# Optimization experiments

Measured on AMD Instinct MI355X. Metric: run time of the kernel, lower is better.

Reference implementation:

```python
import jax, jax.numpy as jnp
import numpy as np

B, N, D_NODE, D_EDGE, D_GRAPH = 2, 1024, 128, 16, 128
MID, OUT = 64, 128


def _linear_params(key, fan_in, fan_out):
    # haiku Linear default: truncated-normal(stddev=1/sqrt(fan_in)) weight, zero bias
    w = jax.random.normal(key, (fan_in, fan_out), dtype=jnp.float32) / np.sqrt(fan_in)
    b = jnp.zeros((fan_out,), dtype=jnp.float32)
    return w, b


def setup_inputs() -> dict:
    key = jax.random.key(0)
    ks = jax.random.split(key, 12)
    features = jax.random.normal(ks[0], (B, N, D_NODE), dtype=jnp.float32)
    e_features = jax.random.normal(ks[1], (B, N, N, D_EDGE), dtype=jnp.float32)
    g_features = jax.random.normal(ks[2], (B, D_GRAPH), dtype=jnp.float32)
    adj = jax.random.randint(ks[3], (B, N, N), 0, 2).astype(jnp.float32)
    # ensure self-loops so every row has at least one valid neighbor
    adj = jnp.maximum(adj, jnp.eye(N, dtype=jnp.float32)[None])
    Wm, bm = _linear_params(ks[4], D_NODE, OUT)
    Wskip, bskip = _linear_params(ks[5], D_NODE, OUT)
    W1, b1 = _linear_params(ks[6], D_NODE, MID)
    W2, b2 = _linear_params(ks[7], D_NODE, MID)
    We, be = _linear_params(ks[8], D_EDGE, MID)
    Wg, bg = _linear_params(ks[9], D_GRAPH, MID)
    Wa, ba = _linear_params(ks[10], MID, 1)
    return dict(features=features, e_features=e_features, g_features=g_features,
                adj=adj, Wm=Wm, bm=bm, Wskip=Wskip, bskip=bskip,
                W1=W1, b1=b1, W2=W2, b2=b2, We=We, be=be, Wg=Wg, bg=bg,
                Wa=Wa, ba=ba)


def reference(features, e_features, g_features, adj,
              Wm, bm, Wskip, bskip, W1, b1, W2, b2, We, be, Wg, bg, Wa, ba):
    # bias mask: 0 where edge exists, -1e9 where not
    bias_mat = (adj - 1.0) * 1e9  # (b,n,n)

    values = features @ Wm + bm          # (b,n,out)
    pre_att_1 = features @ W1 + b1       # (b,n,mid) -> per-target j
    pre_att_2 = features @ W2 + b2       # (b,n,mid) -> per-source i
    pre_att_e = e_features @ We + be     # (b,n,n,mid)
    pre_att_g = g_features @ Wg + bg     # (b,mid)

    # pre_att[b,i,j] = p1[b,j] + p2[b,i] + pe[b,i,j] + pg[b]
    pre_att = (pre_att_1[:, None, :, :] + pre_att_2[:, :, None, :]
               + pre_att_e + pre_att_g[:, None, None, :])  # (b,n,n,mid)

    logits = jnp.squeeze(jax.nn.leaky_relu(pre_att) @ Wa + ba, axis=-1)  # (b,n,n)
    coefs = jax.nn.softmax(logits + bias_mat, axis=-1)                   # (b,n,n)

    ret = jnp.matmul(coefs, values)       # (b,n,out)
    ret = ret + (features @ Wskip + bskip)  # residual
    return jax.nn.relu(ret)               # activation=relu
```

## Files before the change

### kernel.cpp

```cpp
#include <hip/hip_runtime.h>
#include <hip/hip_bf16.h>
#include <cstdint>

#define B_   2
#define N_   1024
#define DN_  128
#define DE_  16
#define DG_  128
#define MID_ 64
#define OUT_ 128
#define TI_  4
#define PR_ROWS 4

typedef short bf16x8 __attribute__((ext_vector_type(8)));
typedef float f32x4  __attribute__((ext_vector_type(4)));

__device__ inline short f2bf(float f) {
    union { float f; unsigned u; } v; v.f = f;
    unsigned r = v.u + 0x7FFFu + ((v.u >> 16) & 1u);
    return (short)(unsigned short)(r >> 16);
}

__device__ inline unsigned pk2(float lo, float hi) {
    union { __hip_bfloat162 h; unsigned u; } p;
    p.h = __float22bfloat162_rn(make_float2(lo, hi));
    return p.u;
}

__global__ void __launch_bounds__(384) prep_all(
    const float* __restrict__ features, const float* __restrict__ g_features,
    const float* __restrict__ Wm, const float* __restrict__ bm,
    const float* __restrict__ Wskip, const float* __restrict__ bskip,
    const float* __restrict__ W1, const float* __restrict__ b1,
    const float* __restrict__ W2, const float* __restrict__ b2,
    const float* __restrict__ We, const float* __restrict__ be,
    const float* __restrict__ Wg, const float* __restrict__ bg,
    float* __restrict__ values, float* __restrict__ skipo,
    float* __restrict__ P1x, float* __restrict__ p2,
    float* __restrict__ pg, short* __restrict__ We_frag)
{
    const int t   = threadIdx.x;
    const int blk = blockIdx.x;

    if (blk == 512) {
        for (int e = t; e < 4 * 64 * 8; e += 384) {
            const int c    = e >> 9;
            const int lane = (e >> 3) & 63;
            const int j    = e & 7;
            const int quad = lane >> 4, s = lane & 15;
            short v = 0;
            if (quad < 2) v = f2bf(We[(quad * 8 + j) * MID_ + c * 16 + s]);
            We_frag[e] = v;
        }
        return;
    }
    if (blk == 513) {
        if (t < MID_) {
            float a0 = bg[t], a1 = bg[t];
            for (int k = 0; k < DG_; ++k) {
                const float w = Wg[k * MID_ + t];
                a0 += g_features[k] * w;
                a1 += g_features[DG_ + k] * w;
            }
            pg[t] = a0; pg[MID_ + t] = a1;
        }
        return;
    }

    const int r0 = blk * PR_ROWS;
    __shared__ float feat[PR_ROWS][DN_];
    for (int idx = t; idx < PR_ROWS * DN_; idx += 384)
        feat[idx >> 7][idx & 127] = features[(size_t)r0 * DN_ + idx];
    __syncthreads();

    const float* W; int c, stride; float base; float* outp; int ostride;
    if (t < 128) {
        W = Wm;    c = t;       stride = OUT_; base = bm[c];
        outp = values + (size_t)r0 * OUT_ + c; ostride = OUT_;
    } else if (t < 256) {
        W = Wskip; c = t - 128; stride = OUT_; base = bskip[c];
        outp = skipo + (size_t)r0 * OUT_ + c;  ostride = OUT_;
    } else if (t < 320) {
        W = W1;    c = t - 256; stride = MID_; base = b1[c] + be[c];
        outp = P1x + (size_t)r0 * MID_ + c;    ostride = MID_;
    } else {
        W = W2;    c = t - 320; stride = MID_; base = b2[c];
        outp = p2 + (size_t)r0 * MID_ + c;     ostride = MID_;
    }

    float acc[PR_ROWS] = {};
    for (int k = 0; k < DN_; ++k) {
        const float w = W[k * stride + c];
        #pragma unroll
        for (int q = 0; q < PR_ROWS; ++q) acc[q] += feat[q][k] * w;
    }
    #pragma unroll
    for (int q = 0; q < PR_ROWS; ++q) outp[q * ostride] = acc[q] + base;
}

__global__ void __launch_bounds__(256) gat_main(
    const float* __restrict__ e_features, const float* __restrict__ adj,
    const short* __restrict__ We_frag, const float* __restrict__ Wa,
    const float* __restrict__ values, const float* __restrict__ skipo,
    const float* __restrict__ P1x, const float* __restrict__ p2,
    const float* __restrict__ pg, float* __restrict__ out)
{
    const int t    = threadIdx.x;
    const int wv   = t >> 6;
    const int l    = t & 63;
    const int quad = l >> 4;
    const int s    = l & 15;
    const int r    = blockIdx.x;
    const int b    = (r >> 2) & 1;
    const int i0   = (((r >> 3) << 2) | (r & 3)) * TI_;

    __shared__ float lgP[TI_][N_];
    __shared__ float redv[TI_][16][36];
    __shared__ float sinv[TI_];

    bf16x8 bfr[4];
    float  wa_r[4], p2i[TI_][4];
    #pragma unroll
    for (int c = 0; c < 4; ++c) {
        bfr[c]  = *(const bf16x8*)&We_frag[(c * 64 + l) * 8];
        wa_r[c] = Wa[c * 16 + s];
        const float pgc = pg[b * MID_ + c * 16 + s];
        #pragma unroll
        for (int ii = 0; ii < TI_; ++ii)
            p2i[ii][c] = p2[((size_t)(b * N_ + i0 + ii)) * MID_ + c * 16 + s] + pgc;
    }
    const size_t erow0 = (size_t)(b * N_ + i0) * N_;

    float4 eA[TI_][2];
    if (quad < 2) {
        #pragma unroll
        for (int ii = 0; ii < TI_; ++ii) {
            const float* ep = &e_features[(erow0 + (size_t)ii * N_ + wv * 16 + s) * DE_ + quad * 8];
            eA[ii][0] = *(const float4*)ep;
            eA[ii][1] = *(const float4*)(ep + 4);
        }
    }
    for (int it = 0; it < 16; ++it) {
        const int tile = wv + it * 4;
        const int j0   = tile * 16;

        unsigned af[TI_][4];
        #pragma unroll
        for (int ii = 0; ii < TI_; ++ii) {
            if (quad < 2) {
                af[ii][0] = pk2(eA[ii][0].x, eA[ii][0].y);
                af[ii][1] = pk2(eA[ii][0].z, eA[ii][0].w);
                af[ii][2] = pk2(eA[ii][1].x, eA[ii][1].y);
                af[ii][3] = pk2(eA[ii][1].z, eA[ii][1].w);
            } else {
                af[ii][0] = af[ii][1] = af[ii][2] = af[ii][3] = 0u;
            }
        }
        if (it < 15) {
            const int jn = (tile + 4) * 16;
            if (quad < 2) {
                #pragma unroll
                for (int ii = 0; ii < TI_; ++ii) {
                    const float* ep = &e_features[(erow0 + (size_t)ii * N_ + jn + s) * DE_ + quad * 8];
                    eA[ii][0] = *(const float4*)ep;
                    eA[ii][1] = *(const float4*)(ep + 4);
                }
            }
        }
        float base[4][4];
        {
            const float* pb = &P1x[((size_t)(b * N_) + j0 + quad * 4) * MID_ + s];
            #pragma unroll
            for (int c = 0; c < 4; ++c)
                #pragma unroll
                for (int rr = 0; rr < 4; ++rr)
                    base[c][rr] = pb[rr * MID_ + c * 16];
        }
        #pragma unroll
        for (int ii = 0; ii < TI_; ++ii) {
            union { unsigned u[4]; bf16x8 v; } a;
            a.u[0] = af[ii][0]; a.u[1] = af[ii][1];
            a.u[2] = af[ii][2]; a.u[3] = af[ii][3];
            f32x4 acc[4];
            #pragma unroll
            for (int c = 0; c < 4; ++c) {
                acc[c] = (f32x4){0.f, 0.f, 0.f, 0.f};
                acc[c] = __builtin_amdgcn_mfma_f32_16x16x32_bf16(a.v, bfr[c], acc[c], 0, 0, 0);
            }
            float tt[4];
            #pragma unroll
            for (int rr = 0; rr < 4; ++rr) {
                float x0 = acc[0][rr] + base[0][rr] + p2i[ii][0];
                float x1 = acc[1][rr] + base[1][rr] + p2i[ii][1];
                float x2 = acc[2][rr] + base[2][rr] + p2i[ii][2];
                float x3 = acc[3][rr] + base[3][rr] + p2i[ii][3];
                x0 = fmaxf(x0, 0.01f * x0);
                x1 = fmaxf(x1, 0.01f * x1);
                x2 = fmaxf(x2, 0.01f * x2);
                x3 = fmaxf(x3, 0.01f * x3);
                tt[rr] = x0 * wa_r[0] + x1 * wa_r[1] + x2 * wa_r[2] + x3 * wa_r[3];
            }
            #pragma unroll
            for (int o = 1; o < 16; o <<= 1) {
                tt[0] += __shfl_xor(tt[0], o);
                tt[1] += __shfl_xor(tt[1], o);
                tt[2] += __shfl_xor(tt[2], o);
                tt[3] += __shfl_xor(tt[3], o);
            }
            if (s < 4) lgP[ii][j0 + quad * 4 + s] = tt[s];
        }
    }
    __syncthreads();

    {
        const size_t arb = (size_t)(b * N_ + i0 + wv) * N_;
        float4 lv[4], av[4];
        #pragma unroll
        for (int q = 0; q < 4; ++q) {
            lv[q] = *(const float4*)&lgP[wv][l * 4 + 256 * q];
            av[q] = *(const float4*)&adj[arb + l * 4 + 256 * q];
        }
        const float NEG = -3.4e38f;
        float m = NEG;
        #pragma unroll
        for (int q = 0; q < 4; ++q) {
            m = fmaxf(m, av[q].x > 0.f ? lv[q].x : NEG);
            m = fmaxf(m, av[q].y > 0.f ? lv[q].y : NEG);
            m = fmaxf(m, av[q].z > 0.f ? lv[q].z : NEG);
            m = fmaxf(m, av[q].w > 0.f ? lv[q].w : NEG);
        }
        #pragma unroll
        for (int o = 1; o < 64; o <<= 1) m = fmaxf(m, __shfl_xor(m, o));
        float sum = 0.f;
        #pragma unroll
        for (int q = 0; q < 4; ++q) {
            float4 e4;
            e4.x = av[q].x > 0.f ? __expf(lv[q].x - m) : 0.f;
            e4.y = av[q].y > 0.f ? __expf(lv[q].y - m) : 0.f;
            e4.z = av[q].z > 0.f ? __expf(lv[q].z - m) : 0.f;
            e4.w = av[q].w > 0.f ? __expf(lv[q].w - m) : 0.f;
            *(float4*)&lgP[wv][l * 4 + 256 * q] = e4;
            sum += (e4.x + e4.y) + (e4.z + e4.w);
        }
        #pragma unroll
        for (int o = 1; o < 64; o <<= 1) sum += __shfl_xor(sum, o);
        if (l == 0) sinv[wv] = 1.0f / sum;
    }
    __syncthreads();

    const int cg = l & 15, jp = l >> 4, ch0 = cg * 8;
    float acc[TI_][8] = {};
    const float* vb = values + (size_t)b * N_ * OUT_ + ch0;
    for (int k = 0; k < 64; ++k) {
        const int j = wv * 4 + jp + k * 16;
        float cw[TI_];
        #pragma unroll
        for (int ii = 0; ii < TI_; ++ii) cw[ii] = lgP[ii][j];
        const float* vp = vb + (size_t)j * OUT_;
        const float4 v0 = *(const float4*)vp;
        const float4 v1 = *(const float4*)(vp + 4);
        const float vv[8] = {v0.x, v0.y, v0.z, v0.w, v1.x, v1.y, v1.z, v1.w};
        #pragma unroll
        for (int ii = 0; ii < TI_; ++ii)
            #pragma unroll
            for (int kk = 0; kk < 8; ++kk)
                acc[ii][kk] += cw[ii] * vv[kk];
    }
    #pragma unroll
    for (int ii = 0; ii < TI_; ++ii)
        #pragma unroll
        for (int kk = 0; kk < 8; ++kk) {
            acc[ii][kk] += __shfl_xor(acc[ii][kk], 16);
            acc[ii][kk] += __shfl_xor(acc[ii][kk], 32);
        }
    if (l < 16) {
        #pragma unroll
        for (int ii = 0; ii < TI_; ++ii)
            #pragma unroll
            for (int q = 0; q < 2; ++q) {
                float4 w4 = make_float4(acc[ii][q * 4], acc[ii][q * 4 + 1],
                                        acc[ii][q * 4 + 2], acc[ii][q * 4 + 3]);
                *(float4*)&redv[wv][l][ii * 8 + q * 4] = w4;
            }
    }
    __syncthreads();
    {
        const int ch = t & 127, g = ch >> 3, kk = ch & 7;
        const int iib = t >> 7;
        #pragma unroll
        for (int p = 0; p < 2; ++p) {
            const int ii = iib + p * 2;
            const float sum = redv[0][g][ii * 8 + kk] + redv[1][g][ii * 8 + kk]
                            + redv[2][g][ii * 8 + kk] + redv[3][g][ii * 8 + kk];
            const size_t ob = ((size_t)(b * N_ + i0 + ii)) * OUT_ + ch;
            out[ob] = fmaxf(sum * sinv[ii] + skipo[ob], 0.f);
        }
    }
}

extern "C" void kernel_launch(void* const* d_in, const int* in_sizes, int n_in,
                              void* d_out, int out_size, void* d_ws, size_t ws_size,
                              hipStream_t stream) {
    const float* features   = (const float*)d_in[0];
    const float* e_features = (const float*)d_in[1];
    const float* g_features = (const float*)d_in[2];
    const float* adj        = (const float*)d_in[3];
    const float* Wm    = (const float*)d_in[4];
    const float* bm    = (const float*)d_in[5];
    const float* Wskip = (const float*)d_in[6];
    const float* bskip = (const float*)d_in[7];
    const float* W1    = (const float*)d_in[8];
    const float* b1    = (const float*)d_in[9];
    const float* W2    = (const float*)d_in[10];
    const float* b2    = (const float*)d_in[11];
    const float* We    = (const float*)d_in[12];
    const float* be    = (const float*)d_in[13];
    const float* Wg    = (const float*)d_in[14];
    const float* bg    = (const float*)d_in[15];
    const float* Wa    = (const float*)d_in[16];
    float* out = (float*)d_out;

    float* ws      = (float*)d_ws;
    float* values  = ws;
    float* skipo   = ws + 262144;
    float* P1x     = ws + 524288;
    float* p2      = ws + 655360;
    float* pg      = ws + 786432;
    short* We_frag = (short*)(ws + 786560);

    prep_all<<<B_ * N_ / PR_ROWS + 2, 384, 0, stream>>>(
        features, g_features, Wm, bm, Wskip, bskip, W1, b1, W2, b2,
        We, be, Wg, bg, values, skipo, P1x, p2, pg, We_frag);
    gat_main<<<B_ * N_ / TI_, 256, 0, stream>>>(
        e_features, adj, We_frag, Wa, values, skipo, P1x, p2, pg, out);
}
```

Measured before the change: 297.9 us.

## Halve rows per block and restructure softmax and aggregation across waves

```diff
diff --git a/kernel.cpp b/kernel.cpp
--- a/kernel.cpp
+++ b/kernel.cpp
@@ -9,7 +9,7 @@
 #define DG_  128
 #define MID_ 64
 #define OUT_ 128
-#define TI_  4
+#define TI_  2
 #define PR_ROWS 4
 
 typedef short bf16x8 __attribute__((ext_vector_type(8)));
@@ -112,11 +112,11 @@
     const int s    = l & 15;
     const int r    = blockIdx.x;
     const int b    = (r >> 2) & 1;
-    const int i0   = (((r >> 3) << 2) | (r & 3)) * TI_;
+    const int i0   = ((((r >> 3) << 2) | (r & 3))) * TI_;
 
     __shared__ float lgP[TI_][N_];
-    __shared__ float redv[TI_][16][36];
-    __shared__ float sinv[TI_];
+    __shared__ float4 redc[TI_][4][32];
+    __shared__ float smax[4], ssum[4];
 
     bf16x8 bfr[4];
     float  wa_r[4], p2i[TI_][4];
@@ -184,20 +184,18 @@
             f32x4 acc[4];
             #pragma unroll
             for (int c = 0; c < 4; ++c) {
-                acc[c] = (f32x4){0.f, 0.f, 0.f, 0.f};
+                #pragma unroll
+                for (int rr = 0; rr < 4; ++rr)
+                    acc[c][rr] = base[c][rr] + p2i[ii][c];
                 acc[c] = __builtin_amdgcn_mfma_f32_16x16x32_bf16(a.v, bfr[c], acc[c], 0, 0, 0);
             }
             float tt[4];
             #pragma unroll
             for (int rr = 0; rr < 4; ++rr) {
-                float x0 = acc[0][rr] + base[0][rr] + p2i[ii][0];
-                float x1 = acc[1][rr] + base[1][rr] + p2i[ii][1];
-                float x2 = acc[2][rr] + base[2][rr] + p2i[ii][2];
-                float x3 = acc[3][rr] + base[3][rr] + p2i[ii][3];
-                x0 = fmaxf(x0, 0.01f * x0);
-                x1 = fmaxf(x1, 0.01f * x1);
-                x2 = fmaxf(x2, 0.01f * x2);
-                x3 = fmaxf(x3, 0.01f * x3);
+                float x0 = acc[0][rr]; x0 = fmaxf(x0, 0.01f * x0);
+                float x1 = acc[1][rr]; x1 = fmaxf(x1, 0.01f * x1);
+                float x2 = acc[2][rr]; x2 = fmaxf(x2, 0.01f * x2);
+                float x3 = acc[3][rr]; x3 = fmaxf(x3, 0.01f * x3);
                 tt[rr] = x0 * wa_r[0] + x1 * wa_r[1] + x2 * wa_r[2] + x3 * wa_r[3];
             }
             #pragma unroll
@@ -213,88 +211,82 @@
     __syncthreads();
 
     {
-        const size_t arb = (size_t)(b * N_ + i0 + wv) * N_;
-        float4 lv[4], av[4];
-        #pragma unroll
-        for (int q = 0; q < 4; ++q) {
-            lv[q] = *(const float4*)&lgP[wv][l * 4 + 256 * q];
-            av[q] = *(const float4*)&adj[arb + l * 4 + 256 * q];
-        }
+        const int tt8 = (t & 127) * 8;
+        const int p   = t >> 7;
+        const size_t arb = (size_t)(b * N_ + i0 + p) * N_;
+        float4 lv0 = *(const float4*)&lgP[p][tt8];
+        float4 lv1 = *(const float4*)&lgP[p][tt8 + 4];
+        float4 av0 = *(const float4*)&adj[arb + tt8];
+        float4 av1 = *(const float4*)&adj[arb + tt8 + 4];
         const float NEG = -3.4e38f;
         float m = NEG;
-        #pragma unroll
-        for (int q = 0; q < 4; ++q) {
-            m = fmaxf(m, av[q].x > 0.f ? lv[q].x : NEG);
-            m = fmaxf(m, av[q].y > 0.f ? lv[q].y : NEG);
-            m = fmaxf(m, av[q].z > 0.f ? lv[q].z : NEG);
-            m = fmaxf(m, av[q].w > 0.f ? lv[q].w : NEG);
-        }
+        m = fmaxf(m, av0.x > 0.f ? lv0.x : NEG);
+        m = fmaxf(m, av0.y > 0.f ? lv0.y : NEG);
+        m = fmaxf(m, av0.z > 0.f ? lv0.z : NEG);
+        m = fmaxf(m, av0.w > 0.f ? lv0.w : NEG);
+        m = fmaxf(m, av1.x > 0.f ? lv1.x : NEG);
+        m = fmaxf(m, av1.y > 0.f ? lv1.y : NEG);
+        m = fmaxf(m, av1.z > 0.f ? lv1.z : NEG);
+        m = fmaxf(m, av1.w > 0.f ? lv1.w : NEG);
         #pragma unroll
         for (int o = 1; o < 64; o <<= 1) m = fmaxf(m, __shfl_xor(m, o));
-        float sum = 0.f;
-        #pragma unroll
-        for (int q = 0; q < 4; ++q) {
-            float4 e4;
-            e4.x = av[q].x > 0.f ? __expf(lv[q].x - m) : 0.f;
-            e4.y = av[q].y > 0.f ? __expf(lv[q].y - m) : 0.f;
-            e4.z = av[q].z > 0.f ? __expf(lv[q].z - m) : 0.f;
-            e4.w = av[q].w > 0.f ? __expf(lv[q].w - m) : 0.f;
-            *(float4*)&lgP[wv][l * 4 + 256 * q] = e4;
-            sum += (e4.x + e4.y) + (e4.z + e4.w);
-        }
+        if (l == 0) smax[wv] = m;
+        __syncthreads();
+        m = fmaxf(smax[p * 2], smax[p * 2 + 1]);
+        float4 e0, e1;
+        e0.x = av0.x > 0.f ? __expf(lv0.x - m) : 0.f;
+        e0.y = av0.y > 0.f ? __expf(lv0.y - m) : 0.f;
+        e0.z = av0.z > 0.f ? __expf(lv0.z - m) : 0.f;
+        e0.w = av0.w > 0.f ? __expf(lv0.w - m) : 0.f;
+        e1.x = av1.x > 0.f ? __expf(lv1.x - m) : 0.f;
+        e1.y = av1.y > 0.f ? __expf(lv1.y - m) : 0.f;
+        e1.z = av1.z > 0.f ? __expf(lv1.z - m) : 0.f;
+        e1.w = av1.w > 0.f ? __expf(lv1.w - m) : 0.f;
+        *(float4*)&lgP[p][tt8]     = e0;
+        *(float4*)&lgP[p][tt8 + 4] = e1;
+        float sum = ((e0.x + e0.y) + (e0.z + e0.w)) + ((e1.x + e1.y) + (e1.z + e1.w));
         #pragma unroll
         for (int o = 1; o < 64; o <<= 1) sum += __shfl_xor(sum, o);
-        if (l == 0) sinv[wv] = 1.0f / sum;
+        if (l == 0) ssum[wv] = sum;
+        __syncthreads();
+    }
+
+    {
+        const int cg = t & 31;
+        const int jp = t >> 5;
+        const float* vb = values + (size_t)b * N_ * OUT_ + cg * 4;
+        float4 a0 = make_float4(0.f, 0.f, 0.f, 0.f);
+        float4 a1 = make_float4(0.f, 0.f, 0.f, 0.f);
+        for (int j = jp; j < N_; j += 8) {
+            const float w0 = lgP[0][j];
+            const float w1 = lgP[1][j];
+            const float4 v = *(const float4*)&vb[(size_t)j * OUT_];
+            a0.x += w0 * v.x; a0.y += w0 * v.y; a0.z += w0 * v.z; a0.w += w0 * v.w;
+            a1.x += w1 * v.x; a1.y += w1 * v.y; a1.z += w1 * v.z; a1.w += w1 * v.w;
+        }
+        a0.x += __shfl_xor(a0.x, 32); a0.y += __shfl_xor(a0.y, 32);
+        a0.z += __shfl_xor(a0.z, 32); a0.w += __shfl_xor(a0.w, 32);
+        a1.x += __shfl_xor(a1.x, 32); a1.y += __shfl_xor(a1.y, 32);
+        a1.z += __shfl_xor(a1.z, 32); a1.w += __shfl_xor(a1.w, 32);
+        if (l < 32) {
+            redc[0][wv][l] = a0;
+            redc[1][wv][l] = a1;
+        }
     }
     __syncthreads();
-
-    const int cg = l & 15, jp = l >> 4, ch0 = cg * 8;
-    float acc[TI_][8] = {};
-    const float* vb = values + (size_t)b * N_ * OUT_ + ch0;
-    for (int k = 0; k < 64; ++k) {
-        const int j = wv * 4 + jp + k * 16;
-        float cw[TI_];
-        #pragma unroll
-        for (int ii = 0; ii < TI_; ++ii) cw[ii] = lgP[ii][j];
-        const float* vp = vb + (size_t)j * OUT_;
-        const float4 v0 = *(const float4*)vp;
-        const float4 v1 = *(const float4*)(vp + 4);
-        const float vv[8] = {v0.x, v0.y, v0.z, v0.w, v1.x, v1.y, v1.z, v1.w};
-        #pragma unroll
-        for (int ii = 0; ii < TI_; ++ii)
-            #pragma unroll
-            for (int kk = 0; kk < 8; ++kk)
-                acc[ii][kk] += cw[ii] * vv[kk];
-    }
-    #pragma unroll
-    for (int ii = 0; ii < TI_; ++ii)
-        #pragma unroll
-        for (int kk = 0; kk < 8; ++kk) {
-            acc[ii][kk] += __shfl_xor(acc[ii][kk], 16);
-            acc[ii][kk] += __shfl_xor(acc[ii][kk], 32);
-        }
-    if (l < 16) {
-        #pragma unroll
-        for (int ii = 0; ii < TI_; ++ii)
-            #pragma unroll
-            for (int q = 0; q < 2; ++q) {
-                float4 w4 = make_float4(acc[ii][q * 4], acc[ii][q * 4 + 1],
-                                        acc[ii][q * 4 + 2], acc[ii][q * 4 + 3]);
-                *(float4*)&redv[wv][l][ii * 8 + q * 4] = w4;
-            }
-    }
-    __syncthreads();
-    {
-        const int ch = t & 127, g = ch >> 3, kk = ch & 7;
-        const int iib = t >> 7;
-        #pragma unroll
-        for (int p = 0; p < 2; ++p) {
-            const int ii = iib + p * 2;
-            const float sum = redv[0][g][ii * 8 + kk] + redv[1][g][ii * 8 + kk]
-                            + redv[2][g][ii * 8 + kk] + redv[3][g][ii * 8 + kk];
-            const size_t ob = ((size_t)(b * N_ + i0 + ii)) * OUT_ + ch;
-            out[ob] = fmaxf(sum * sinv[ii] + skipo[ob], 0.f);
-        }
+    if (t < 64) {
+        const int ch4 = t & 31, p = t >> 5;
+        const float4 r0 = redc[p][0][ch4], r1 = redc[p][1][ch4];
+        const float4 r2 = redc[p][2][ch4], r3 = redc[p][3][ch4];
+        const float inv = 1.0f / (ssum[p * 2] + ssum[p * 2 + 1]);
+        const size_t ob = ((size_t)(b * N_ + i0 + p)) * OUT_ + ch4 * 4;
+        const float4 sk = *(const float4*)&skipo[ob];
+        float4 o;
+        o.x = fmaxf((r0.x + r1.x + r2.x + r3.x) * inv + sk.x, 0.f);
+        o.y = fmaxf((r0.y + r1.y + r2.y + r3.y) * inv + sk.y, 0.f);
+        o.z = fmaxf((r0.z + r1.z + r2.z + r3.z) * inv + sk.z, 0.f);
+        o.w = fmaxf((r0.w + r1.w + r2.w + r3.w) * inv + sk.w, 0.f);
+        *(float4*)&out[ob] = o;
     }
 }
 
```

New measurement: 349.4 us. 1.17x slower.

## Double gat_main block to 512 threads, splitting tiles and softmax across 8 waves

Applied to the files above, without the earlier changes.

```diff
diff --git a/kernel.cpp b/kernel.cpp
--- a/kernel.cpp
+++ b/kernel.cpp
@@ -98,7 +98,7 @@
     for (int q = 0; q < PR_ROWS; ++q) outp[q * ostride] = acc[q] + base;
 }
 
-__global__ void __launch_bounds__(256) gat_main(
+__global__ void __launch_bounds__(512, 4) gat_main(
     const float* __restrict__ e_features, const float* __restrict__ adj,
     const short* __restrict__ We_frag, const float* __restrict__ Wa,
     const float* __restrict__ values, const float* __restrict__ skipo,
@@ -115,8 +115,8 @@
     const int i0   = (((r >> 3) << 2) | (r & 3)) * TI_;
 
     __shared__ float lgP[TI_][N_];
-    __shared__ float redv[TI_][16][36];
-    __shared__ float sinv[TI_];
+    __shared__ float redv[8][16][36];
+    __shared__ float smax[8], ssum[8];
 
     bf16x8 bfr[4];
     float  wa_r[4], p2i[TI_][4];
@@ -140,8 +140,8 @@
             eA[ii][1] = *(const float4*)(ep + 4);
         }
     }
-    for (int it = 0; it < 16; ++it) {
-        const int tile = wv + it * 4;
+    for (int it = 0; it < 8; ++it) {
+        const int tile = wv + it * 8;
         const int j0   = tile * 16;
 
         unsigned af[TI_][4];
@@ -156,8 +156,8 @@
                 af[ii][0] = af[ii][1] = af[ii][2] = af[ii][3] = 0u;
             }
         }
-        if (it < 15) {
-            const int jn = (tile + 4) * 16;
+        if (it < 7) {
+            const int jn = (tile + 8) * 16;
             if (quad < 2) {
                 #pragma unroll
                 for (int ii = 0; ii < TI_; ++ii) {
@@ -184,20 +184,18 @@
             f32x4 acc[4];
             #pragma unroll
             for (int c = 0; c < 4; ++c) {
-                acc[c] = (f32x4){0.f, 0.f, 0.f, 0.f};
+                #pragma unroll
+                for (int rr = 0; rr < 4; ++rr)
+                    acc[c][rr] = base[c][rr] + p2i[ii][c];
                 acc[c] = __builtin_amdgcn_mfma_f32_16x16x32_bf16(a.v, bfr[c], acc[c], 0, 0, 0);
             }
             float tt[4];
             #pragma unroll
             for (int rr = 0; rr < 4; ++rr) {
-                float x0 = acc[0][rr] + base[0][rr] + p2i[ii][0];
-                float x1 = acc[1][rr] + base[1][rr] + p2i[ii][1];
-                float x2 = acc[2][rr] + base[2][rr] + p2i[ii][2];
-                float x3 = acc[3][rr] + base[3][rr] + p2i[ii][3];
-                x0 = fmaxf(x0, 0.01f * x0);
-                x1 = fmaxf(x1, 0.01f * x1);
-                x2 = fmaxf(x2, 0.01f * x2);
-                x3 = fmaxf(x3, 0.01f * x3);
+                float x0 = acc[0][rr]; x0 = fmaxf(x0, 0.01f * x0);
+                float x1 = acc[1][rr]; x1 = fmaxf(x1, 0.01f * x1);
+                float x2 = acc[2][rr]; x2 = fmaxf(x2, 0.01f * x2);
+                float x3 = acc[3][rr]; x3 = fmaxf(x3, 0.01f * x3);
                 tt[rr] = x0 * wa_r[0] + x1 * wa_r[1] + x2 * wa_r[2] + x3 * wa_r[3];
             }
             #pragma unroll
@@ -213,88 +211,96 @@
     __syncthreads();
 
     {
-        const size_t arb = (size_t)(b * N_ + i0 + wv) * N_;
-        float4 lv[4], av[4];
-        #pragma unroll
-        for (int q = 0; q < 4; ++q) {
-            lv[q] = *(const float4*)&lgP[wv][l * 4 + 256 * q];
-            av[q] = *(const float4*)&adj[arb + l * 4 + 256 * q];
-        }
+        const int p = wv & 3, h = wv >> 2;
+        const int o8 = h * 512 + l * 8;
+        const size_t arb = (size_t)(b * N_ + i0 + p) * N_;
+        float4 lv0 = *(const float4*)&lgP[p][o8];
+        float4 lv1 = *(const float4*)&lgP[p][o8 + 4];
+        float4 av0 = *(const float4*)&adj[arb + o8];
+        float4 av1 = *(const float4*)&adj[arb + o8 + 4];
         const float NEG = -3.4e38f;
         float m = NEG;
-        #pragma unroll
-        for (int q = 0; q < 4; ++q) {
-            m = fmaxf(m, av[q].x > 0.f ? lv[q].x : NEG);
-            m = fmaxf(m, av[q].y > 0.f ? lv[q].y : NEG);
-            m = fmaxf(m, av[q].z > 0.f ? lv[q].z : NEG);
-            m = fmaxf(m, av[q].w > 0.f ? lv[q].w : NEG);
-        }
+        m = fmaxf(m, av0.x > 0.f ? lv0.x : NEG);
+        m = fmaxf(m, av0.y > 0.f ? lv0.y : NEG);
+        m = fmaxf(m, av0.z > 0.f ? lv0.z : NEG);
+        m = fmaxf(m, av0.w > 0.f ? lv0.w : NEG);
+        m = fmaxf(m, av1.x > 0.f ? lv1.x : NEG);
+        m = fmaxf(m, av1.y > 0.f ? lv1.y : NEG);
+        m = fmaxf(m, av1.z > 0.f ? lv1.z : NEG);
+        m = fmaxf(m, av1.w > 0.f ? lv1.w : NEG);
         #pragma unroll
         for (int o = 1; o < 64; o <<= 1) m = fmaxf(m, __shfl_xor(m, o));
-        float sum = 0.f;
-        #pragma unroll
-        for (int q = 0; q < 4; ++q) {
-            float4 e4;
-            e4.x = av[q].x > 0.f ? __expf(lv[q].x - m) : 0.f;
-            e4.y = av[q].y > 0.f ? __expf(lv[q].y - m) : 0.f;
-            e4.z = av[q].z > 0.f ? __expf(lv[q].z - m) : 0.f;
-            e4.w = av[q].w > 0.f ? __expf(lv[q].w - m) : 0.f;
-            *(float4*)&lgP[wv][l * 4 + 256 * q] = e4;
-            sum += (e4.x + e4.y) + (e4.z + e4.w);
-        }
+        if (l == 0) smax[wv] = m;
+        __syncthreads();
+        m = fmaxf(smax[p], smax[p + 4]);
+        float4 e0, e1;
+        e0.x = av0.x > 0.f ? __expf(lv0.x - m) : 0.f;
+        e0.y = av0.y > 0.f ? __expf(lv0.y - m) : 0.f;
+        e0.z = av0.z > 0.f ? __expf(lv0.z - m) : 0.f;
+        e0.w = av0.w > 0.f ? __expf(lv0.w - m) : 0.f;
+        e1.x = av1.x > 0.f ? __expf(lv1.x - m) : 0.f;
+        e1.y = av1.y > 0.f ? __expf(lv1.y - m) : 0.f;
+        e1.z = av1.z > 0.f ? __expf(lv1.z - m) : 0.f;
+        e1.w = av1.w > 0.f ? __expf(lv1.w - m) : 0.f;
+        *(float4*)&lgP[p][o8]     = e0;
+        *(float4*)&lgP[p][o8 + 4] = e1;
+        float sum = ((e0.x + e0.y) + (e0.z + e0.w)) + ((e1.x + e1.y) + (e1.z + e1.w));
         #pragma unroll
         for (int o = 1; o < 64; o <<= 1) sum += __shfl_xor(sum, o);
-        if (l == 0) sinv[wv] = 1.0f / sum;
-    }
-    __syncthreads();
-
-    const int cg = l & 15, jp = l >> 4, ch0 = cg * 8;
-    float acc[TI_][8] = {};
-    const float* vb = values + (size_t)b * N_ * OUT_ + ch0;
-    for (int k = 0; k < 64; ++k) {
-        const int j = wv * 4 + jp + k * 16;
-        float cw[TI_];
-        #pragma unroll
-        for (int ii = 0; ii < TI_; ++ii) cw[ii] = lgP[ii][j];
-        const float* vp = vb + (size_t)j * OUT_;
-        const float4 v0 = *(const float4*)vp;
-        const float4 v1 = *(const float4*)(vp + 4);
-        const float vv[8] = {v0.x, v0.y, v0.z, v0.w, v1.x, v1.y, v1.z, v1.w};
+        if (l == 0) ssum[wv] = sum;
+        __syncthreads();
+    }
+
+    {
+        const int cg  = l & 15;
+        const int jp  = (wv << 2) | (l >> 4);
+        const int ch0 = cg * 8;
+        float acc[TI_][8] = {};
+        const float* vb = values + (size_t)b * N_ * OUT_ + ch0;
+        for (int k = 0; k < 32; ++k) {
+            const int j = jp + k * 32;
+            float cw[TI_];
+            #pragma unroll
+            for (int ii = 0; ii < TI_; ++ii) cw[ii] = lgP[ii][j];
+            const float* vp = vb + (size_t)j * OUT_;
+            const float4 v0 = *(const float4*)vp;
+            const float4 v1 = *(const float4*)(vp + 4);
+            const float vv[8] = {v0.x, v0.y, v0.z, v0.w, v1.x, v1.y, v1.z, v1.w};
+            #pragma unroll
+            for (int ii = 0; ii < TI_; ++ii)
+                #pragma unroll
+                for (int kk = 0; kk < 8; ++kk)
+                    acc[ii][kk] += cw[ii] * vv[kk];
+        }
         #pragma unroll
         for (int ii = 0; ii < TI_; ++ii)
             #pragma unroll
-            for (int kk = 0; kk < 8; ++kk)
-                acc[ii][kk] += cw[ii] * vv[kk];
-    }
-    #pragma unroll
-    for (int ii = 0; ii < TI_; ++ii)
-        #pragma unroll
-        for (int kk = 0; kk < 8; ++kk) {
-            acc[ii][kk] += __shfl_xor(acc[ii][kk], 16);
-            acc[ii][kk] += __shfl_xor(acc[ii][kk], 32);
-        }
-    if (l < 16) {
-        #pragma unroll
-        for (int ii = 0; ii < TI_; ++ii)
-            #pragma unroll
-            for (int q = 0; q < 2; ++q) {
-                float4 w4 = make_float4(acc[ii][q * 4], acc[ii][q * 4 + 1],
-                                        acc[ii][q * 4 + 2], acc[ii][q * 4 + 3]);
-                *(float4*)&redv[wv][l][ii * 8 + q * 4] = w4;
-            }
+            for (int kk = 0; kk < 8; ++kk) {
+                acc[ii][kk] += __shfl_xor(acc[ii][kk], 16);
+                acc[ii][kk] += __shfl_xor(acc[ii][kk], 32);
+            }
+        if (l < 16) {
+            #pragma unroll
+            for (int ii = 0; ii < TI_; ++ii)
+                #pragma unroll
+                for (int q = 0; q < 2; ++q) {
+                    float4 w4 = make_float4(acc[ii][q * 4], acc[ii][q * 4 + 1],
+                                            acc[ii][q * 4 + 2], acc[ii][q * 4 + 3]);
+                    *(float4*)&redv[wv][l][ii * 8 + q * 4] = w4;
+                }
+        }
     }
     __syncthreads();
     {
-        const int ch = t & 127, g = ch >> 3, kk = ch & 7;
-        const int iib = t >> 7;
-        #pragma unroll
-        for (int p = 0; p < 2; ++p) {
-            const int ii = iib + p * 2;
-            const float sum = redv[0][g][ii * 8 + kk] + redv[1][g][ii * 8 + kk]
-                            + redv[2][g][ii * 8 + kk] + redv[3][g][ii * 8 + kk];
-            const size_t ob = ((size_t)(b * N_ + i0 + ii)) * OUT_ + ch;
-            out[ob] = fmaxf(sum * sinv[ii] + skipo[ob], 0.f);
-        }
+        const int ii = t >> 7;
+        const int ch = t & 127;
+        const int g  = ch >> 3, kk = ch & 7;
+        float sum = 0.f;
+        #pragma unroll
+        for (int w = 0; w < 8; ++w) sum += redv[w][g][ii * 8 + kk];
+        const float inv = 1.0f / (ssum[ii] + ssum[ii + 4]);
+        const size_t ob = ((size_t)(b * N_ + i0 + ii)) * OUT_ + ch;
+        out[ob] = fmaxf(sum * inv + skipo[ob], 0.f);
     }
 }
 
@@ -331,6 +337,6 @@
     prep_all<<<B_ * N_ / PR_ROWS + 2, 384, 0, stream>>>(
         features, g_features, Wm, bm, Wskip, bskip, W1, b1, W2, b2,
         We, be, Wg, bg, values, skipo, P1x, p2, pg, We_frag);
-    gat_main<<<B_ * N_ / TI_, 256, 0, stream>>>(
+    gat_main<<<B_ * N_ / TI_, 512, 0, stream>>>(
         e_features, adj, We_frag, Wa, values, skipo, P1x, p2, pg, out);
 }
```

Measured after the change: 429.9 us. +44.3%, slower.

## Split GAT into logits kernel with 4x more blocks and separate softmax-aggregate kernel

Applied to the files above, without the earlier changes.

```diff
diff --git a/kernel.cpp b/kernel.cpp
--- a/kernel.cpp
+++ b/kernel.cpp
@@ -98,7 +98,231 @@
     for (int q = 0; q < PR_ROWS; ++q) outp[q * ostride] = acc[q] + base;
 }
 
-__global__ void __launch_bounds__(256) gat_main(
+__global__ void __launch_bounds__(256) gat_logits(
+    const float* __restrict__ e_features, const float* __restrict__ adj,
+    const short* __restrict__ We_frag, const float* __restrict__ Wa,
+    const float* __restrict__ P1x, const float* __restrict__ p2,
+    const float* __restrict__ pg, float* __restrict__ lgG)
+{
+    const int t     = threadIdx.x;
+    const int wv    = t >> 6;
+    const int l     = t & 63;
+    const int quad  = l >> 4;
+    const int s     = l & 15;
+    const int r     = blockIdx.x;
+    const int jc    = r & 3;
+    const int b     = (r >> 2) & 1;
+    const int i0    = (r >> 3) * TI_;
+    const int jbase = jc * 256;
+
+    __shared__ float lgL[TI_][256];
+
+    bf16x8 bfr[4];
+    float  wa_r[4], p2i[TI_][4];
+    #pragma unroll
+    for (int c = 0; c < 4; ++c) {
+        bfr[c]  = *(const bf16x8*)&We_frag[(c * 64 + l) * 8];
+        wa_r[c] = Wa[c * 16 + s];
+        const float pgc = pg[b * MID_ + c * 16 + s];
+        #pragma unroll
+        for (int ii = 0; ii < TI_; ++ii)
+            p2i[ii][c] = p2[((size_t)(b * N_ + i0 + ii)) * MID_ + c * 16 + s] + pgc;
+    }
+    const size_t erow0 = (size_t)(b * N_ + i0) * N_;
+
+    float4 eA[TI_][2];
+    if (quad < 2) {
+        #pragma unroll
+        for (int ii = 0; ii < TI_; ++ii) {
+            const float* ep = &e_features[(erow0 + (size_t)ii * N_ + jbase + wv * 16 + s) * DE_ + quad * 8];
+            eA[ii][0] = *(const float4*)ep;
+            eA[ii][1] = *(const float4*)(ep + 4);
+        }
+    }
+    for (int it = 0; it < 4; ++it) {
+        const int j0 = jbase + (wv + it * 4) * 16;
+
+        unsigned af[TI_][4];
+        #pragma unroll
+        for (int ii = 0; ii < TI_; ++ii) {
+            if (quad < 2) {
+                af[ii][0] = pk2(eA[ii][0].x, eA[ii][0].y);
+                af[ii][1] = pk2(eA[ii][0].z, eA[ii][0].w);
+                af[ii][2] = pk2(eA[ii][1].x, eA[ii][1].y);
+                af[ii][3] = pk2(eA[ii][1].z, eA[ii][1].w);
+            } else {
+                af[ii][0] = af[ii][1] = af[ii][2] = af[ii][3] = 0u;
+            }
+        }
+        if (it < 3) {
+            const int jn = jbase + (wv + (it + 1) * 4) * 16;
+            if (quad < 2) {
+                #pragma unroll
+                for (int ii = 0; ii < TI_; ++ii) {
+                    const float* ep = &e_features[(erow0 + (size_t)ii * N_ + jn + s) * DE_ + quad * 8];
+                    eA[ii][0] = *(const float4*)ep;
+                    eA[ii][1] = *(const float4*)(ep + 4);
+                }
+            }
+        }
+        float base[4][4];
+        {
+            const float* pb = &P1x[((size_t)(b * N_) + j0 + quad * 4) * MID_ + s];
+            #pragma unroll
+            for (int c = 0; c < 4; ++c)
+                #pragma unroll
+                for (int rr = 0; rr < 4; ++rr)
+                    base[c][rr] = pb[rr * MID_ + c * 16];
+        }
+        #pragma unroll
+        for (int ii = 0; ii < TI_; ++ii) {
+            union { unsigned u[4]; bf16x8 v; } a;
+            a.u[0] = af[ii][0]; a.u[1] = af[ii][1];
+            a.u[2] = af[ii][2]; a.u[3] = af[ii][3];
+            f32x4 acc[4];
+            #pragma unroll
+            for (int c = 0; c < 4; ++c) {
+                #pragma unroll
+                for (int rr = 0; rr < 4; ++rr)
+                    acc[c][rr] = base[c][rr] + p2i[ii][c];
+                acc[c] = __builtin_amdgcn_mfma_f32_16x16x32_bf16(a.v, bfr[c], acc[c], 0, 0, 0);
+            }
+            float tt[4];
+            #pragma unroll
+            for (int rr = 0; rr < 4; ++rr) {
+                float x0 = acc[0][rr]; x0 = fmaxf(x0, 0.01f * x0);
+                float x1 = acc[1][rr]; x1 = fmaxf(x1, 0.01f * x1);
+                float x2 = acc[2][rr]; x2 = fmaxf(x2, 0.01f * x2);
+                float x3 = acc[3][rr]; x3 = fmaxf(x3, 0.01f * x3);
+                tt[rr] = x0 * wa_r[0] + x1 * wa_r[1] + x2 * wa_r[2] + x3 * wa_r[3];
+            }
+            #pragma unroll
+            for (int o = 1; o < 16; o <<= 1) {
+                tt[0] += __shfl_xor(tt[0], o);
+                tt[1] += __shfl_xor(tt[1], o);
+                tt[2] += __shfl_xor(tt[2], o);
+                tt[3] += __shfl_xor(tt[3], o);
+            }
+            if (s < 4) lgL[ii][j0 - jbase + quad * 4 + s] = tt[s];
+        }
+    }
+    __syncthreads();
+
+    {
+        const int   ii  = t >> 6;
+        const int   jl  = (t & 63) * 4;
+        const size_t row = (size_t)(b * N_ + i0 + ii);
+        float4 lg4 = make_float4(lgL[ii][jl], lgL[ii][jl + 1],
+                                 lgL[ii][jl + 2], lgL[ii][jl + 3]);
+        const float4 a4 = *(const float4*)&adj[row * N_ + jbase + jl];
+        const float NEG = -3.4e38f;
+        lg4.x = a4.x > 0.f ? lg4.x : NEG;
+        lg4.y = a4.y > 0.f ? lg4.y : NEG;
+        lg4.z = a4.z > 0.f ? lg4.z : NEG;
+        lg4.w = a4.w > 0.f ? lg4.w : NEG;
+        *(float4*)&lgG[row * N_ + jbase + jl] = lg4;
+    }
+}
+
+__global__ void __launch_bounds__(256) gat_out(
+    const float* __restrict__ lgG, const float* __restrict__ values,
+    const float* __restrict__ skipo, float* __restrict__ out)
+{
+    const int t  = threadIdx.x;
+    const int wv = t >> 6;
+    const int l  = t & 63;
+    const int r  = blockIdx.x;
+    const int b  = (r >> 2) & 1;
+    const int i0 = (((r >> 3) << 2) | (r & 3)) * TI_;
+
+    __shared__ float lgP[TI_][N_];
+    __shared__ float redv[4][16][36];
+    __shared__ float sinv[TI_];
+
+    #pragma unroll
+    for (int ii = 0; ii < TI_; ++ii)
+        *(float4*)&lgP[ii][t * 4] =
+            *(const float4*)&lgG[(size_t)(b * N_ + i0 + ii) * N_ + t * 4];
+    __syncthreads();
+
+    {
+        float v[16];
+        float m = -3.4e38f;
+        #pragma unroll
+        for (int q = 0; q < 16; ++q) {
+            v[q] = lgP[wv][l + 64 * q];
+            m = fmaxf(m, v[q]);
+        }
+        #pragma unroll
+        for (int o = 1; o < 64; o <<= 1) m = fmaxf(m, __shfl_xor(m, o));
+        float sum = 0.f;
+        #pragma unroll
+        for (int q = 0; q < 16; ++q) {
+            const float e = __expf(v[q] - m);
+            lgP[wv][l + 64 * q] = e;
+            sum += e;
+        }
+        #pragma unroll
+        for (int o = 1; o < 64; o <<= 1) sum += __shfl_xor(sum, o);
+        if (l == 0) sinv[wv] = 1.0f / sum;
+    }
+    __syncthreads();
+
+    {
+        const int cg  = l & 15;
+        const int jp  = (wv << 2) | (l >> 4);
+        const int ch0 = cg * 8;
+        float acc[TI_][8] = {};
+        const float* vb = values + (size_t)b * N_ * OUT_ + ch0;
+        #pragma unroll 2
+        for (int k = 0; k < 64; ++k) {
+            const int j = jp + k * 16;
+            float cw[TI_];
+            #pragma unroll
+            for (int ii = 0; ii < TI_; ++ii) cw[ii] = lgP[ii][j];
+            const float* vp = vb + (size_t)j * OUT_;
+            const float4 v0 = *(const float4*)vp;
+            const float4 v1 = *(const float4*)(vp + 4);
+            const float vv[8] = {v0.x, v0.y, v0.z, v0.w, v1.x, v1.y, v1.z, v1.w};
+            #pragma unroll
+            for (int ii = 0; ii < TI_; ++ii)
+                #pragma unroll
+                for (int kk = 0; kk < 8; ++kk)
+                    acc[ii][kk] += cw[ii] * vv[kk];
+        }
+        #pragma unroll
+        for (int ii = 0; ii < TI_; ++ii)
+            #pragma unroll
+            for (int kk = 0; kk < 8; ++kk) {
+                acc[ii][kk] += __shfl_xor(acc[ii][kk], 16);
+                acc[ii][kk] += __shfl_xor(acc[ii][kk], 32);
+            }
+        if (l < 16) {
+            #pragma unroll
+            for (int ii = 0; ii < TI_; ++ii)
+                #pragma unroll
+                for (int q = 0; q < 2; ++q) {
+                    float4 w4 = make_float4(acc[ii][q * 4], acc[ii][q * 4 + 1],
+                                            acc[ii][q * 4 + 2], acc[ii][q * 4 + 3]);
+                    *(float4*)&redv[wv][l][ii * 8 + q * 4] = w4;
+                }
+        }
+    }
+    __syncthreads();
+    {
+        const int ch = t & 127, g = ch >> 3, kk = ch & 7;
+        #pragma unroll
+        for (int p = 0; p < 2; ++p) {
+            const int ii = (t >> 7) + 2 * p;
+            const float sum = redv[0][g][ii * 8 + kk] + redv[1][g][ii * 8 + kk]
+                            + redv[2][g][ii * 8 + kk] + redv[3][g][ii * 8 + kk];
+            const size_t ob = ((size_t)(b * N_ + i0 + ii)) * OUT_ + ch;
+            out[ob] = fmaxf(sum * sinv[ii] + skipo[ob], 0.f);
+        }
+    }
+}
+
+__global__ void __launch_bounds__(256) gat_fused(
     const float* __restrict__ e_features, const float* __restrict__ adj,
     const short* __restrict__ We_frag, const float* __restrict__ Wa,
     const float* __restrict__ values, const float* __restrict__ skipo,
@@ -115,7 +339,7 @@
     const int i0   = (((r >> 3) << 2) | (r & 3)) * TI_;
 
     __shared__ float lgP[TI_][N_];
-    __shared__ float redv[TI_][16][36];
+    __shared__ float redv[4][16][36];
     __shared__ float sinv[TI_];
 
     bf16x8 bfr[4];
@@ -141,9 +365,7 @@
         }
     }
     for (int it = 0; it < 16; ++it) {
-        const int tile = wv + it * 4;
-        const int j0   = tile * 16;
-
+        const int j0 = (wv + it * 4) * 16;
         unsigned af[TI_][4];
         #pragma unroll
         for (int ii = 0; ii < TI_; ++ii) {
@@ -157,7 +379,7 @@
             }
         }
         if (it < 15) {
-            const int jn = (tile + 4) * 16;
+            const int jn = (wv + (it + 1) * 4) * 16;
             if (quad < 2) {
                 #pragma unroll
                 for (int ii = 0; ii < TI_; ++ii) {
@@ -184,20 +406,18 @@
             f32x4 acc[4];
             #pragma unroll
             for (int c = 0; c < 4; ++c) {
-                acc[c] = (f32x4){0.f, 0.f, 0.f, 0.f};
+                #pragma unroll
+                for (int rr = 0; rr < 4; ++rr)
+                    acc[c][rr] = base[c][rr] + p2i[ii][c];
                 acc[c] = __builtin_amdgcn_mfma_f32_16x16x32_bf16(a.v, bfr[c], acc[c], 0, 0, 0);
             }
             float tt[4];
             #pragma unroll
             for (int rr = 0; rr < 4; ++rr) {
-                float x0 = acc[0][rr] + base[0][rr] + p2i[ii][0];
-                float x1 = acc[1][rr] + base[1][rr] + p2i[ii][1];
-                float x2 = acc[2][rr] + base[2][rr] + p2i[ii][2];
-                float x3 = acc[3][rr] + base[3][rr] + p2i[ii][3];
-                x0 = fmaxf(x0, 0.01f * x0);
-                x1 = fmaxf(x1, 0.01f * x1);
-                x2 = fmaxf(x2, 0.01f * x2);
-                x3 = fmaxf(x3, 0.01f * x3);
+                float x0 = acc[0][rr]; x0 = fmaxf(x0, 0.01f * x0);
+                float x1 = acc[1][rr]; x1 = fmaxf(x1, 0.01f * x1);
+                float x2 = acc[2][rr]; x2 = fmaxf(x2, 0.01f * x2);
+                float x3 = acc[3][rr]; x3 = fmaxf(x3, 0.01f * x3);
                 tt[rr] = x0 * wa_r[0] + x1 * wa_r[1] + x2 * wa_r[2] + x3 * wa_r[3];
             }
             #pragma unroll
@@ -214,33 +434,23 @@
 
     {
         const size_t arb = (size_t)(b * N_ + i0 + wv) * N_;
-        float4 lv[4], av[4];
-        #pragma unroll
-        for (int q = 0; q < 4; ++q) {
-            lv[q] = *(const float4*)&lgP[wv][l * 4 + 256 * q];
-            av[q] = *(const float4*)&adj[arb + l * 4 + 256 * q];
-        }
-        const float NEG = -3.4e38f;
-        float m = NEG;
-        #pragma unroll
-        for (int q = 0; q < 4; ++q) {
-            m = fmaxf(m, av[q].x > 0.f ? lv[q].x : NEG);
-            m = fmaxf(m, av[q].y > 0.f ? lv[q].y : NEG);
-            m = fmaxf(m, av[q].z > 0.f ? lv[q].z : NEG);
-            m = fmaxf(m, av[q].w > 0.f ? lv[q].w : NEG);
+        float v[16];
+        float m = -3.4e38f;
+        #pragma unroll
+        for (int q = 0; q < 16; ++q) {
+            const float av = adj[arb + l + 64 * q];
+            const float lv = lgP[wv][l + 64 * q];
+            v[q] = av > 0.f ? lv : -3.4e38f;
+            m = fmaxf(m, v[q]);
         }
         #pragma unroll
         for (int o = 1; o < 64; o <<= 1) m = fmaxf(m, __shfl_xor(m, o));
         float sum = 0.f;
         #pragma unroll
-        for (int q = 0; q < 4; ++q) {
-            float4 e4;
-            e4.x = av[q].x > 0.f ? __expf(lv[q].x - m) : 0.f;
-            e4.y = av[q].y > 0.f ? __expf(lv[q].y - m) : 0.f;
-            e4.z = av[q].z > 0.f ? __expf(lv[q].z - m) : 0.f;
-            e4.w = av[q].w > 0.f ? __expf(lv[q].w - m) : 0.f;
-            *(float4*)&lgP[wv][l * 4 + 256 * q] = e4;
-            sum += (e4.x + e4.y) + (e4.z + e4.w);
+        for (int q = 0; q < 16; ++q) {
+            const float e = __expf(v[q] - m);
+            lgP[wv][l + 64 * q] = e;
+            sum += e;
         }
         #pragma unroll
         for (int o = 1; o < 64; o <<= 1) sum += __shfl_xor(sum, o);
@@ -248,48 +458,52 @@
     }
     __syncthreads();
 
-    const int cg = l & 15, jp = l >> 4, ch0 = cg * 8;
-    float acc[TI_][8] = {};
-    const float* vb = values + (size_t)b * N_ * OUT_ + ch0;
-    for (int k = 0; k < 64; ++k) {
-        const int j = wv * 4 + jp + k * 16;
-        float cw[TI_];
-        #pragma unroll
-        for (int ii = 0; ii < TI_; ++ii) cw[ii] = lgP[ii][j];
-        const float* vp = vb + (size_t)j * OUT_;
-        const float4 v0 = *(const float4*)vp;
-        const float4 v1 = *(const float4*)(vp + 4);
-        const float vv[8] = {v0.x, v0.y, v0.z, v0.w, v1.x, v1.y, v1.z, v1.w};
+    {
+        const int cg  = l & 15;
+        const int jp  = (wv << 2) | (l >> 4);
+        const int ch0 = cg * 8;
+        float acc[TI_][8] = {};
+        const float* vb = values + (size_t)b * N_ * OUT_ + ch0;
+        #pragma unroll 2
+        for (int k = 0; k < 64; ++k) {
+            const int j = jp + k * 16;
+            float cw[TI_];
+            #pragma unroll
+            for (int ii = 0; ii < TI_; ++ii) cw[ii] = lgP[ii][j];
+            const float* vp = vb + (size_t)j * OUT_;
+            const float4 v0 = *(const float4*)vp;
+            const float4 v1 = *(const float4*)(vp + 4);
+            const float vv[8] = {v0.x, v0.y, v0.z, v0.w, v1.x, v1.y, v1.z, v1.w};
+            #pragma unroll
+            for (int ii = 0; ii < TI_; ++ii)
+                #pragma unroll
+                for (int kk = 0; kk < 8; ++kk)
+                    acc[ii][kk] += cw[ii] * vv[kk];
+        }
         #pragma unroll
         for (int ii = 0; ii < TI_; ++ii)
             #pragma unroll
-            for (int kk = 0; kk < 8; ++kk)
-                acc[ii][kk] += cw[ii] * vv[kk];
-    }
-    #pragma unroll
-    for (int ii = 0; ii < TI_; ++ii)
-        #pragma unroll
-        for (int kk = 0; kk < 8; ++kk) {
-            acc[ii][kk] += __shfl_xor(acc[ii][kk], 16);
-            acc[ii][kk] += __shfl_xor(acc[ii][kk], 32);
-        }
-    if (l < 16) {
-        #pragma unroll
-        for (int ii = 0; ii < TI_; ++ii)
-            #pragma unroll
-            for (int q = 0; q < 2; ++q) {
-                float4 w4 = make_float4(acc[ii][q * 4], acc[ii][q * 4 + 1],
-                                        acc[ii][q * 4 + 2], acc[ii][q * 4 + 3]);
-                *(float4*)&redv[wv][l][ii * 8 + q * 4] = w4;
-            }
+            for (int kk = 0; kk < 8; ++kk) {
+                acc[ii][kk] += __shfl_xor(acc[ii][kk], 16);
+                acc[ii][kk] += __shfl_xor(acc[ii][kk], 32);
+            }
+        if (l < 16) {
+            #pragma unroll
+            for (int ii = 0; ii < TI_; ++ii)
+                #pragma unroll
+                for (int q = 0; q < 2; ++q) {
+                    float4 w4 = make_float4(acc[ii][q * 4], acc[ii][q * 4 + 1],
+                                            acc[ii][q * 4 + 2], acc[ii][q * 4 + 3]);
+                    *(float4*)&redv[wv][l][ii * 8 + q * 4] = w4;
+                }
+        }
     }
     __syncthreads();
     {
         const int ch = t & 127, g = ch >> 3, kk = ch & 7;
-        const int iib = t >> 7;
         #pragma unroll
         for (int p = 0; p < 2; ++p) {
-            const int ii = iib + p * 2;
+            const int ii = (t >> 7) + 2 * p;
             const float sum = redv[0][g][ii * 8 + kk] + redv[1][g][ii * 8 + kk]
                             + redv[2][g][ii * 8 + kk] + redv[3][g][ii * 8 + kk];
             const size_t ob = ((size_t)(b * N_ + i0 + ii)) * OUT_ + ch;
@@ -327,10 +541,19 @@
     float* p2      = ws + 655360;
     float* pg      = ws + 786432;
     short* We_frag = (short*)(ws + 786560);
+    float* lgG     = ws + 787584;
 
     prep_all<<<B_ * N_ / PR_ROWS + 2, 384, 0, stream>>>(
         features, g_features, Wm, bm, Wskip, bskip, W1, b1, W2, b2,
         We, be, Wg, bg, values, skipo, P1x, p2, pg, We_frag);
-    gat_main<<<B_ * N_ / TI_, 256, 0, stream>>>(
-        e_features, adj, We_frag, Wa, values, skipo, P1x, p2, pg, out);
-}
+
+    const size_t need = (size_t)(787584 + B_ * N_ * N_) * sizeof(float);
+    if (ws_size >= need) {
+        gat_logits<<<B_ * N_ / TI_ * 4, 256, 0, stream>>>(
+            e_features, adj, We_frag, Wa, P1x, p2, pg, lgG);
+        gat_out<<<B_ * N_ / TI_, 256, 0, stream>>>(lgG, values, skipo, out);
+    } else {
+        gat_fused<<<B_ * N_ / TI_, 256, 0, stream>>>(
+            e_features, adj, We_frag, Wa, values, skipo, P1x, p2, pg, out);
+    }
+}
```

Result: slower. 306.3 us (+2.8%).
